# Optimization experiments

Measured on AMD Instinct MI355X. Metric: run time of the kernel, lower is better.

Reference implementation:

```python
import jax, jax.numpy as jnp
import numpy as np

BETA = 0.25
K, D = 1024, 64


def setup_inputs() -> dict:
    key = jax.random.key(0)
    k1, k2 = jax.random.split(key)
    z = jax.random.normal(k1, (2, D, 32, 32, 32), dtype=jnp.float32)
    # nn.Embedding initialized uniform(-1/K, 1/K)
    embedding = jax.random.uniform(k2, (K, D), dtype=jnp.float32,
                                   minval=-1.0 / K, maxval=1.0 / K)
    return {"z": z, "embedding": embedding}


def reference(z, embedding):
    # z: [B, D, X, Y, Z] -> [B, X, Y, Z, D]
    zp = jnp.transpose(z, (0, 2, 3, 4, 1))
    latents_shape = zp.shape
    flat = zp.reshape(-1, embedding.shape[1])  # [N, D]

    dist = (jnp.sum(flat ** 2, axis=1, keepdims=True)
            + jnp.sum(embedding ** 2, axis=1)
            - 2.0 * flat @ embedding.T)
    min_encoding_indices = jnp.argmin(dist, axis=1)  # [N]

    z_q = embedding[min_encoding_indices].reshape(latents_shape)

    commitment_loss = jnp.mean((jax.lax.stop_gradient(z_q) - zp) ** 2)
    embedding_loss = jnp.mean((z_q - jax.lax.stop_gradient(zp)) ** 2)
    vq_loss = commitment_loss * BETA + embedding_loss  # point=False branch

    # straight-through estimator
    z_q_st = zp + jax.lax.stop_gradient(z_q - zp)
    out = jnp.transpose(z_q_st, (0, 4, 1, 2, 3))  # back to [B, D, X, Y, Z]
    return out, vq_loss, min_encoding_indices[:, None]
```

## Files before the change

kernel.cpp:

```cpp
#include <hip/hip_runtime.h>
#include <hip/hip_fp16.h>

#define KDIM 1024
#define DDIM 64
#define SPAT 32768
#define NVEC 65536
#define DSP  (DDIM * SPAT)
#define MARGIN 5.0e-4f
#define ZPAD 69
#define QCAP 1536

typedef _Float16 half8 __attribute__((ext_vector_type(8)));
typedef float floatx4 __attribute__((ext_vector_type(4)));

__device__ __forceinline__ float opaque(float x) { asm volatile("" : "+v"(x)); return x; }

__device__ __forceinline__ float np_sumsq64(const float* x) {
    float r8[8];
#pragma unroll
    for (int j = 0; j < 8; ++j) r8[j] = opaque(x[1 + j] * x[1 + j]);
#pragma unroll
    for (int i = 8; i < 56; i += 8) {
#pragma unroll
        for (int j = 0; j < 8; ++j) r8[j] += opaque(x[1 + i + j] * x[1 + i + j]);
    }
    float res = ((r8[0] + r8[1]) + (r8[2] + r8[3])) + ((r8[4] + r8[5]) + (r8[6] + r8[7]));
#pragma unroll
    for (int m = 57; m < 64; ++m) res += opaque(x[m] * x[m]);
    return opaque(x[0] * x[0]) + res;
}

__global__ void vq_prep_e(const float* __restrict__ emb, float* __restrict__ e2,
                          float* __restrict__ h, __half* __restrict__ eh,
                          float* __restrict__ loss) {
    const int tid = threadIdx.x;
    const int kbase = blockIdx.x * 16;
#pragma unroll
    for (int i = 0; i < 4; ++i) {
        int g = i * 256 + tid;
        float v = emb[(size_t)kbase * DDIM + g];
        e2[(size_t)kbase * DDIM + g] = v + v;
        eh[(size_t)kbase * DDIM + g] = (__half)(_Float16)(v * 1024.0f);
    }
    if (tid < 16) h[kbase + tid] = np_sumsq64(emb + (size_t)(kbase + tid) * DDIM);
    if (blockIdx.x == 0 && tid == 0) *loss = 0.f;
}

__global__ __launch_bounds__(256, 4) void vq_mfma_kernel(
    const float* __restrict__ z, const float* __restrict__ emb,
    const __half* __restrict__ eh_, const float* __restrict__ h_,
    const float* __restrict__ e2_, float* __restrict__ out,
    float* __restrict__ loss, float* __restrict__ idxf)
{
    __shared__ float zrow[64 * ZPAD];
    __shared__ float lds_sn[64];
    __shared__ float Lm1[16][64];
    __shared__ float m1f[64];
    __shared__ int   qcnt;
    __shared__ unsigned short      qk[QCAP];
    __shared__ unsigned char       qn[QCAP];
    __shared__ unsigned long long  qres[QCAP];

    const int tid = threadIdx.x, l = tid & 63, w = tid >> 6;
    const int nbase = blockIdx.x * 64;
    const int b = nbase >> 15, s0 = nbase & (SPAT - 1);
    const int col16 = l & 15, g16 = l >> 4;
    const float* zbase = z + (size_t)b * DSP + s0;

    if (tid == 0) qcnt = 0;

    {
        const int dbase = w * 16;
#pragma unroll
        for (int j = 0; j < 16; ++j)
            zrow[l * ZPAD + dbase + j] = zbase[(size_t)(dbase + j) * SPAT + l];
    }
    __syncthreads();

    if (tid < 64) lds_sn[tid] = np_sumsq64(&zrow[tid * ZPAD]);

    half8 zf[4][2];
#pragma unroll
    for (int nc = 0; nc < 4; ++nc) {
        const int r = nc * 16 + col16;
#pragma unroll
        for (int kp = 0; kp < 2; ++kp) {
            const int d0 = g16 * 8 + kp * 32;
            half8 vh;
#pragma unroll
            for (int u = 0; u < 8; ++u)
                vh[u] = (_Float16)zrow[r * ZPAD + d0 + u];
            zf[nc][kp] = vh;
        }
    }
    __syncthreads();

    float snv[4];
#pragma unroll
    for (int nc = 0; nc < 4; ++nc) snv[nc] = lds_sn[nc * 16 + col16];

    const int myk0 = w * 256;

    float m1[4];
#pragma unroll
    for (int nc = 0; nc < 4; ++nc) m1[nc] = 3.0e38f;
    {
        size_t eoff = (size_t)(myk0 + col16) * DDIM + g16 * 8;
        half8 ef0 = *(const half8*)(eh_ + eoff);
        half8 ef1 = *(const half8*)(eh_ + eoff + 32);
        floatx4 hv = *(const floatx4*)(h_ + myk0 + g16 * 4);
        for (int t = 0; t < 16; ++t) {
            half8 cf0 = ef0, cf1 = ef1; floatx4 chv = hv;
            if (t < 15) {
                const size_t e2off = (size_t)(myk0 + (t + 1) * 16 + col16) * DDIM + g16 * 8;
                ef0 = *(const half8*)(eh_ + e2off);
                ef1 = *(const half8*)(eh_ + e2off + 32);
                hv  = *(const floatx4*)(h_ + myk0 + (t + 1) * 16 + g16 * 4);
            }
#pragma unroll
            for (int nc = 0; nc < 4; ++nc) {
                floatx4 acc = {0.f, 0.f, 0.f, 0.f};
                acc = __builtin_amdgcn_mfma_f32_16x16x32_f16(cf0, zf[nc][0], acc, 0, 0, 0);
                acc = __builtin_amdgcn_mfma_f32_16x16x32_f16(cf1, zf[nc][1], acc, 0, 0, 0);
#pragma unroll
                for (int j = 0; j < 4; ++j) {
                    float dist = fmaf(-0.001953125f, acc[j], snv[nc] + chv[j]);
                    m1[nc] = fminf(m1[nc], dist);
                }
            }
        }
    }
    const int slot = w * 4 + g16;
#pragma unroll
    for (int nc = 0; nc < 4; ++nc) Lm1[slot][nc * 16 + col16] = m1[nc];
    __syncthreads();

    if (tid < 64) {
        float M1 = Lm1[0][tid];
#pragma unroll
        for (int sI = 1; sI < 16; ++sI) M1 = fminf(M1, Lm1[sI][tid]);
        m1f[tid] = M1;
    }
    __syncthreads();

    float thr[4];
#pragma unroll
    for (int nc = 0; nc < 4; ++nc) thr[nc] = m1f[nc * 16 + col16] + MARGIN;
    {
        size_t eoff = (size_t)(myk0 + col16) * DDIM + g16 * 8;
        half8 ef0 = *(const half8*)(eh_ + eoff);
        half8 ef1 = *(const half8*)(eh_ + eoff + 32);
        floatx4 hv = *(const floatx4*)(h_ + myk0 + g16 * 4);
        for (int t = 0; t < 16; ++t) {
            half8 cf0 = ef0, cf1 = ef1; floatx4 chv = hv;
            if (t < 15) {
                const size_t e2off = (size_t)(myk0 + (t + 1) * 16 + col16) * DDIM + g16 * 8;
                ef0 = *(const half8*)(eh_ + e2off);
                ef1 = *(const half8*)(eh_ + e2off + 32);
                hv  = *(const floatx4*)(h_ + myk0 + (t + 1) * 16 + g16 * 4);
            }
            const int rbase = myk0 + t * 16 + g16 * 4;
#pragma unroll
            for (int nc = 0; nc < 4; ++nc) {
                floatx4 acc = {0.f, 0.f, 0.f, 0.f};
                acc = __builtin_amdgcn_mfma_f32_16x16x32_f16(cf0, zf[nc][0], acc, 0, 0, 0);
                acc = __builtin_amdgcn_mfma_f32_16x16x32_f16(cf1, zf[nc][1], acc, 0, 0, 0);
#pragma unroll
                for (int j = 0; j < 4; ++j) {
                    float dist = fmaf(-0.001953125f, acc[j], snv[nc] + chv[j]);
                    if (dist <= thr[nc]) {
                        int p = atomicAdd(&qcnt, 1);
                        if (p < QCAP) {
                            qk[p] = (unsigned short)(rbase + j);
                            qn[p] = (unsigned char)(nc * 16 + col16);
                        }
                    }
                }
            }
        }
    }
    __syncthreads();

    const int qlen = min(qcnt, QCAP);

    for (int i = tid; i < qlen; i += 256) {
        const int k = qk[i], r = qn[i];
        const float* zr = &zrow[r * ZPAD];
        const floatx4* ep = (const floatx4*)(e2_ + (size_t)k * DDIM);
        float acc = 0.f;
#pragma unroll
        for (int dq = 0; dq < 16; ++dq) {
            floatx4 v = ep[dq];
            acc = fmaf(v[0], zr[4 * dq + 0], acc);
            acc = fmaf(v[1], zr[4 * dq + 1], acc);
            acc = fmaf(v[2], zr[4 * dq + 2], acc);
            acc = fmaf(v[3], zr[4 * dq + 3], acc);
        }
        float tt   = lds_sn[r] + h_[k];
        float dist = tt - acc;
        unsigned int db = __float_as_uint(dist);
        qres[i] = ((unsigned long long)db << 32) | (unsigned int)k;
    }
    __syncthreads();

    if (tid < 64) {
        unsigned long long best = ~0ull;
        for (int i = 0; i < qlen; ++i)
            if (qn[i] == tid) best = min(best, qres[i]);
        const int I1 = (int)(best & 0xffffffffu);
        const int n = nbase + tid;
        idxf[n] = (float)I1;

        const float* e = emb + (size_t)I1 * DDIM;
        float* op = out + (size_t)b * DSP + s0 + tid;
        float lsum = 0.f;
#pragma unroll
        for (int d = 0; d < DDIM; ++d) {
            float qv = e[d];
            op[(size_t)d * SPAT] = qv;
            float df = qv - zrow[tid * ZPAD + d];
            lsum = fmaf(df, df, lsum);
        }
#pragma unroll
        for (int off = 32; off > 0; off >>= 1)
            lsum += __shfl_down(lsum, off, 64);
        if (tid == 0)
            atomicAdd(loss, lsum * (1.25f / 4194304.0f));
    }
}

extern "C" void kernel_launch(void* const* d_in, const int* in_sizes, int n_in,
                              void* d_out, int out_size, void* d_ws, size_t ws_size,
                              hipStream_t stream) {
    const float* z   = (const float*)d_in[0];
    const float* emb = (const float*)d_in[1];
    float* out  = (float*)d_out;
    float* loss = out + 4194304;
    float* idxf = out + 4194305;

    float* h_  = (float*)d_ws;
    float* e2_ = h_ + KDIM;
    __half* eh_ = (__half*)(e2_ + KDIM * DDIM);

    vq_prep_e<<<KDIM / 16, 256, 0, stream>>>(emb, e2_, h_, eh_, loss);
    vq_mfma_kernel<<<NVEC / 64, 256, 0, stream>>>(z, emb, eh_, h_, e2_, out, loss, idxf);
}
```

Before: 66.06 us.

## Switch distance GEMM to 32x32x16 MFMA tiles and stage codebook norms in LDS

Replaces the 16x16x32 MFMA tiling with 32x32x16 MFMA over two 32-row z tiles, four K-steps each, so every wave covers 32 codes per step instead of 16. The codebook norms are staged once into shared memory rather than read from global in the inner loop, and the per-wave min reduction slots shrink from 16 to 8. The aim is fewer MFMA issues and fewer global loads per distance tile. In exchange it uses more accumulator registers, and the occupancy bound drops from 4 to 3 blocks per CU.

```diff
diff --git a/kernel.cpp b/kernel.cpp
--- a/kernel.cpp
+++ b/kernel.cpp
@@ -12,6 +12,7 @@
 
 typedef _Float16 half8 __attribute__((ext_vector_type(8)));
 typedef float floatx4 __attribute__((ext_vector_type(4)));
+typedef float floatx16 __attribute__((ext_vector_type(16)));
 
 __device__ __forceinline__ float opaque(float x) { asm volatile("" : "+v"(x)); return x; }
 
@@ -46,7 +47,7 @@
     if (blockIdx.x == 0 && tid == 0) *loss = 0.f;
 }
 
-__global__ __launch_bounds__(256, 4) void vq_mfma_kernel(
+__global__ __launch_bounds__(256, 3) void vq_mfma_kernel(
     const float* __restrict__ z, const float* __restrict__ emb,
     const __half* __restrict__ eh_, const float* __restrict__ h_,
     const float* __restrict__ e2_, float* __restrict__ out,
@@ -54,7 +55,8 @@
 {
     __shared__ float zrow[64 * ZPAD];
     __shared__ float lds_sn[64];
-    __shared__ float Lm1[16][64];
+    __shared__ float h_lds[KDIM];
+    __shared__ float Lm1[8][64];
     __shared__ float m1f[64];
     __shared__ int   qcnt;
     __shared__ unsigned short      qk[QCAP];
@@ -64,11 +66,12 @@
     const int tid = threadIdx.x, l = tid & 63, w = tid >> 6;
     const int nbase = blockIdx.x * 64;
     const int b = nbase >> 15, s0 = nbase & (SPAT - 1);
-    const int col16 = l & 15, g16 = l >> 4;
+    const int l31 = l & 31, half = l >> 5;
     const float* zbase = z + (size_t)b * DSP + s0;
 
     if (tid == 0) qcnt = 0;
 
+    ((float4*)h_lds)[tid] = ((const float4*)h_)[tid];
     {
         const int dbase = w * 16;
 #pragma unroll
@@ -79,106 +82,106 @@
 
     if (tid < 64) lds_sn[tid] = np_sumsq64(&zrow[tid * ZPAD]);
 
-    half8 zf[4][2];
-#pragma unroll
-    for (int nc = 0; nc < 4; ++nc) {
-        const int r = nc * 16 + col16;
-#pragma unroll
-        for (int kp = 0; kp < 2; ++kp) {
-            const int d0 = g16 * 8 + kp * 32;
+    half8 zf[2][4];
+#pragma unroll
+    for (int tile = 0; tile < 2; ++tile) {
+#pragma unroll
+        for (int c = 0; c < 4; ++c) {
+            const int base = (tile * 32 + l31) * ZPAD + c * 16 + half * 8;
             half8 vh;
 #pragma unroll
             for (int u = 0; u < 8; ++u)
-                vh[u] = (_Float16)zrow[r * ZPAD + d0 + u];
-            zf[nc][kp] = vh;
-        }
-    }
-    __syncthreads();
-
-    float snv[4];
-#pragma unroll
-    for (int nc = 0; nc < 4; ++nc) snv[nc] = lds_sn[nc * 16 + col16];
+                vh[u] = (_Float16)zrow[base + u];
+            zf[tile][c] = vh;
+        }
+    }
+    __syncthreads();
+
+    float snv[2] = {lds_sn[l31], lds_sn[32 + l31]};
 
     const int myk0 = w * 256;
 
-    float m1[4];
-#pragma unroll
-    for (int nc = 0; nc < 4; ++nc) m1[nc] = 3.0e38f;
+    half8 ef0, ef1, ef2, ef3;
+#define LOADA(t) { \
+        const size_t o_ = (size_t)(myk0 + (t) * 32 + l31) * DDIM + half * 8; \
+        ef0 = *(const half8*)(eh_ + o_); \
+        ef1 = *(const half8*)(eh_ + o_ + 16); \
+        ef2 = *(const half8*)(eh_ + o_ + 32); \
+        ef3 = *(const half8*)(eh_ + o_ + 48); }
+
+    float m1[2] = {3.0e38f, 3.0e38f};
+    LOADA(0)
+    for (int t = 0; t < 8; ++t) {
+        half8 cf0 = ef0, cf1 = ef1, cf2 = ef2, cf3 = ef3;
+        if (t < 7) LOADA(t + 1)
+        floatx4 hq[4];
+#pragma unroll
+        for (int q = 0; q < 4; ++q)
+            hq[q] = *(const floatx4*)(&h_lds[myk0 + t * 32 + q * 8 + half * 4]);
+#pragma unroll
+        for (int tile = 0; tile < 2; ++tile) {
+            floatx16 acc = {};
+            acc = __builtin_amdgcn_mfma_f32_32x32x16_f16(cf0, zf[tile][0], acc, 0, 0, 0);
+            acc = __builtin_amdgcn_mfma_f32_32x32x16_f16(cf1, zf[tile][1], acc, 0, 0, 0);
+            acc = __builtin_amdgcn_mfma_f32_32x32x16_f16(cf2, zf[tile][2], acc, 0, 0, 0);
+            acc = __builtin_amdgcn_mfma_f32_32x32x16_f16(cf3, zf[tile][3], acc, 0, 0, 0);
+#pragma unroll
+            for (int q = 0; q < 4; ++q)
+#pragma unroll
+                for (int e = 0; e < 4; ++e) {
+                    float dist = fmaf(-0.001953125f, acc[q * 4 + e], snv[tile] + hq[q][e]);
+                    m1[tile] = fminf(m1[tile], dist);
+                }
+        }
+    }
     {
-        size_t eoff = (size_t)(myk0 + col16) * DDIM + g16 * 8;
-        half8 ef0 = *(const half8*)(eh_ + eoff);
-        half8 ef1 = *(const half8*)(eh_ + eoff + 32);
-        floatx4 hv = *(const floatx4*)(h_ + myk0 + g16 * 4);
-        for (int t = 0; t < 16; ++t) {
-            half8 cf0 = ef0, cf1 = ef1; floatx4 chv = hv;
-            if (t < 15) {
-                const size_t e2off = (size_t)(myk0 + (t + 1) * 16 + col16) * DDIM + g16 * 8;
-                ef0 = *(const half8*)(eh_ + e2off);
-                ef1 = *(const half8*)(eh_ + e2off + 32);
-                hv  = *(const floatx4*)(h_ + myk0 + (t + 1) * 16 + g16 * 4);
-            }
-#pragma unroll
-            for (int nc = 0; nc < 4; ++nc) {
-                floatx4 acc = {0.f, 0.f, 0.f, 0.f};
-                acc = __builtin_amdgcn_mfma_f32_16x16x32_f16(cf0, zf[nc][0], acc, 0, 0, 0);
-                acc = __builtin_amdgcn_mfma_f32_16x16x32_f16(cf1, zf[nc][1], acc, 0, 0, 0);
-#pragma unroll
-                for (int j = 0; j < 4; ++j) {
-                    float dist = fmaf(-0.001953125f, acc[j], snv[nc] + chv[j]);
-                    m1[nc] = fminf(m1[nc], dist);
-                }
-            }
-        }
-    }
-    const int slot = w * 4 + g16;
-#pragma unroll
-    for (int nc = 0; nc < 4; ++nc) Lm1[slot][nc * 16 + col16] = m1[nc];
+        const int slot = w * 2 + half;
+        Lm1[slot][l31]      = m1[0];
+        Lm1[slot][32 + l31] = m1[1];
+    }
     __syncthreads();
 
     if (tid < 64) {
         float M1 = Lm1[0][tid];
 #pragma unroll
-        for (int sI = 1; sI < 16; ++sI) M1 = fminf(M1, Lm1[sI][tid]);
+        for (int sI = 1; sI < 8; ++sI) M1 = fminf(M1, Lm1[sI][tid]);
         m1f[tid] = M1;
     }
     __syncthreads();
 
-    float thr[4];
-#pragma unroll
-    for (int nc = 0; nc < 4; ++nc) thr[nc] = m1f[nc * 16 + col16] + MARGIN;
-    {
-        size_t eoff = (size_t)(myk0 + col16) * DDIM + g16 * 8;
-        half8 ef0 = *(const half8*)(eh_ + eoff);
-        half8 ef1 = *(const half8*)(eh_ + eoff + 32);
-        floatx4 hv = *(const floatx4*)(h_ + myk0 + g16 * 4);
-        for (int t = 0; t < 16; ++t) {
-            half8 cf0 = ef0, cf1 = ef1; floatx4 chv = hv;
-            if (t < 15) {
-                const size_t e2off = (size_t)(myk0 + (t + 1) * 16 + col16) * DDIM + g16 * 8;
-                ef0 = *(const half8*)(eh_ + e2off);
-                ef1 = *(const half8*)(eh_ + e2off + 32);
-                hv  = *(const floatx4*)(h_ + myk0 + (t + 1) * 16 + g16 * 4);
-            }
-            const int rbase = myk0 + t * 16 + g16 * 4;
-#pragma unroll
-            for (int nc = 0; nc < 4; ++nc) {
-                floatx4 acc = {0.f, 0.f, 0.f, 0.f};
-                acc = __builtin_amdgcn_mfma_f32_16x16x32_f16(cf0, zf[nc][0], acc, 0, 0, 0);
-                acc = __builtin_amdgcn_mfma_f32_16x16x32_f16(cf1, zf[nc][1], acc, 0, 0, 0);
-#pragma unroll
-                for (int j = 0; j < 4; ++j) {
-                    float dist = fmaf(-0.001953125f, acc[j], snv[nc] + chv[j]);
-                    if (dist <= thr[nc]) {
+    float thr[2] = {m1f[l31] + MARGIN, m1f[32 + l31] + MARGIN};
+    LOADA(0)
+    for (int t = 0; t < 8; ++t) {
+        half8 cf0 = ef0, cf1 = ef1, cf2 = ef2, cf3 = ef3;
+        if (t < 7) LOADA(t + 1)
+        floatx4 hq[4];
+#pragma unroll
+        for (int q = 0; q < 4; ++q)
+            hq[q] = *(const floatx4*)(&h_lds[myk0 + t * 32 + q * 8 + half * 4]);
+        const int kstep = myk0 + t * 32 + half * 4;
+#pragma unroll
+        for (int tile = 0; tile < 2; ++tile) {
+            floatx16 acc = {};
+            acc = __builtin_amdgcn_mfma_f32_32x32x16_f16(cf0, zf[tile][0], acc, 0, 0, 0);
+            acc = __builtin_amdgcn_mfma_f32_32x32x16_f16(cf1, zf[tile][1], acc, 0, 0, 0);
+            acc = __builtin_amdgcn_mfma_f32_32x32x16_f16(cf2, zf[tile][2], acc, 0, 0, 0);
+            acc = __builtin_amdgcn_mfma_f32_32x32x16_f16(cf3, zf[tile][3], acc, 0, 0, 0);
+#pragma unroll
+            for (int q = 0; q < 4; ++q)
+#pragma unroll
+                for (int e = 0; e < 4; ++e) {
+                    float dist = fmaf(-0.001953125f, acc[q * 4 + e], snv[tile] + hq[q][e]);
+                    if (dist <= thr[tile]) {
                         int p = atomicAdd(&qcnt, 1);
                         if (p < QCAP) {
-                            qk[p] = (unsigned short)(rbase + j);
-                            qn[p] = (unsigned char)(nc * 16 + col16);
+                            qk[p] = (unsigned short)(kstep + q * 8 + e);
+                            qn[p] = (unsigned char)(tile * 32 + l31);
                         }
                     }
                 }
-            }
-        }
-    }
+        }
+    }
+#undef LOADA
     __syncthreads();
 
     const int qlen = min(qcnt, QCAP);
```

New measurement: 76.19 us. 15.3% more time.
